# Kernel optimization log

Hardware: AMD Instinct MI355X
Metric: run time of the kernel (lower is better)

## Reference

```python
import jax, jax.numpy as jnp
import numpy as np

N_NODES = 50000
N_EDGES = 800000
D_IN = 128
D_HID = 128
N_LAYERS = 3
BN_EPS = 1e-5


def setup_inputs() -> dict:
    key = jax.random.key(0)
    ks = jax.random.split(key, 12)
    x = jax.random.normal(ks[0], (N_NODES, D_IN), dtype=jnp.float32)
    edge_index = jax.random.randint(ks[1], (2, N_EDGES), 0, N_NODES, dtype=jnp.int64)
    edge_weight = jax.random.uniform(ks[2], (N_EDGES,), dtype=jnp.float32)
    s1 = 1.0 / np.sqrt(D_IN)
    s2 = 1.0 / np.sqrt(D_HID)
    # stacked per-layer GIN MLP params (layer 0 in_dim == hidden_dim so stacking is valid)
    W1s = jax.random.uniform(ks[3], (N_LAYERS, D_HID, D_HID), jnp.float32, -s1, s1)
    b1s = jax.random.uniform(ks[4], (N_LAYERS, D_HID), jnp.float32, -s1, s1)
    W2s = jax.random.uniform(ks[5], (N_LAYERS, D_HID, D_HID), jnp.float32, -s2, s2)
    b2s = jax.random.uniform(ks[6], (N_LAYERS, D_HID), jnp.float32, -s2, s2)
    eps = jnp.zeros((N_LAYERS,), jnp.float32)  # GINConv eps init 0
    gamma = jnp.ones((D_HID,), jnp.float32)
    beta = jnp.zeros((D_HID,), jnp.float32)
    Wp = jax.random.uniform(ks[7], (D_HID, D_HID), jnp.float32, -s2, s2)
    bp = jax.random.uniform(ks[8], (D_HID,), jnp.float32, -s2, s2)
    prelu_a = jnp.asarray(0.25, jnp.float32)
    return {"x": x, "edge_weight": edge_weight, "W1s": W1s, "b1s": b1s,
            "W2s": W2s, "b2s": b2s, "eps": eps, "gamma": gamma, "beta": beta,
            "Wp": Wp, "bp": bp, "prelu_a": prelu_a, "edge_index": edge_index}


def reference(x, edge_weight, W1s, b1s, W2s, b2s, eps, gamma, beta, Wp, bp, prelu_a, edge_index):
    src, dst = edge_index[0], edge_index[1]
    z = x
    for i in range(N_LAYERS):
        # GINConv: sum-aggregate weighted neighbor messages, then 2-layer MLP
        msg = z[src] * edge_weight[:, None]                       # [E, d]
        agg = jax.ops.segment_sum(msg, dst, num_segments=N_NODES)  # [N, d]
        h = (1.0 + eps[i]) * z + agg
        h = jax.nn.relu(h @ W1s[i] + b1s[i]) @ W2s[i] + b2s[i]
        z = jax.nn.relu(h)  # activation; dropout inactive (eval)
    # BatchNorm1d (training-mode batch statistics, biased variance)
    mean = jnp.mean(z, axis=0)
    var = jnp.var(z, axis=0)
    zn = (z - mean) * jax.lax.rsqrt(var + BN_EPS) * gamma + beta
    # projection head: Linear -> PReLU (dropout inactive)
    p = zn @ Wp + bp
    p = jnp.where(p >= 0, p, prelu_a * p)
    return zn, p
```

## Files before the change

kernel.cpp:

```cpp
#include <hip/hip_runtime.h>
#include <hip/hip_fp16.h>

#define N_NODES 50000
#define N_EDGES 800000
#define D 128
#define ND (N_NODES * D)
#define BN_EPS 1e-5f

typedef short bf16x8 __attribute__((ext_vector_type(8)));
typedef float f32x4 __attribute__((ext_vector_type(4)));
typedef unsigned short u16x8 __attribute__((ext_vector_type(8)));

__device__ inline unsigned short f2bf(float f) {
    unsigned int u = __float_as_uint(f);
    u += 0x7FFF + ((u >> 16) & 1);
    return (unsigned short)(u >> 16);
}
__device__ inline float bf2f(unsigned short h) {
    return __uint_as_float(((unsigned int)h) << 16);
}
__device__ inline unsigned short f2h(float f) {
    return __half_as_ushort(__float2half(f));
}
__device__ inline float h2f(unsigned short u) {
    return __half2float(__ushort_as_half(u));
}

__global__ void convert_x(const float* __restrict__ x, ushort* __restrict__ xh) {
    int i = (blockIdx.x * blockDim.x + threadIdx.x) * 4;
    if (i < ND) {
        float4 v = *(const float4*)(x + i);
        *(ushort4*)(xh + i) = make_ushort4(f2h(v.x), f2h(v.y), f2h(v.z), f2h(v.w));
    }
}

__global__ void pack_w_split(const float* __restrict__ W1s, const float* __restrict__ W2s,
                             const float* __restrict__ Wp, ushort* __restrict__ out) {
    int idx = blockIdx.x * blockDim.x + threadIdx.x;
    if (idx >= 7 * 16384) return;
    int m = idx >> 14;
    int p = idx & 16383;
    int c = p >> 11;
    int kc = (p >> 9) & 3;
    int lane = (p >> 3) & 63;
    int j = p & 7;
    int k = kc * 32 + (lane >> 4) * 8 + j;
    int col = c * 16 + (lane & 15);
    const float* src = (m < 3) ? (W1s + (size_t)m * 16384)
                     : (m < 6) ? (W2s + (size_t)(m - 3) * 16384)
                               : Wp;
    float v = src[k * 128 + col];
    unsigned short hi = f2bf(v);
    float r = v - bf2f(hi);
    out[(size_t)(2 * m) * 16384 + p] = hi;
    out[(size_t)(2 * m + 1) * 16384 + p] = f2bf(r);
}

__global__ void hist_kernel(const int* __restrict__ dst, int* __restrict__ offs) {
    int e = blockIdx.x * blockDim.x + threadIdx.x;
    if (e < N_EDGES) atomicAdd(&offs[dst[e] + 1], 1);
}

__global__ void scan_kernel(int* __restrict__ offs, int* __restrict__ cursor) {
    __shared__ int wsum[16];
    __shared__ int carry_s;
    int tid = threadIdx.x;
    int lane = tid & 63;
    int wave = tid >> 6;
    if (tid == 0) { carry_s = 0; cursor[0] = 0; }
    __syncthreads();
    for (int base = 1; base <= N_NODES; base += 8192) {
        int i0 = base + tid * 8;
        int v[8];
        #pragma unroll
        for (int k = 0; k < 8; ++k) {
            int idx = i0 + k;
            v[k] = (idx <= N_NODES) ? offs[idx] : 0;
        }
        #pragma unroll
        for (int k = 1; k < 8; ++k) v[k] += v[k - 1];
        int tsum = v[7];
        int x = tsum;
        #pragma unroll
        for (int d = 1; d < 64; d <<= 1) {
            int y = __shfl_up(x, d, 64);
            if (lane >= d) x += y;
        }
        if (lane == 63) wsum[wave] = x;
        __syncthreads();
        if (wave == 0 && lane < 16) {
            int y = wsum[lane];
            #pragma unroll
            for (int d = 1; d < 16; d <<= 1) {
                int t = __shfl_up(y, d, 64);
                if (lane >= d) y += t;
            }
            wsum[lane] = y;
        }
        __syncthreads();
        int waveoff = (wave > 0) ? wsum[wave - 1] : 0;
        int total = wsum[15];
        int add = (x - tsum) + waveoff + carry_s;
        #pragma unroll
        for (int k = 0; k < 8; ++k) {
            int idx = i0 + k;
            if (idx <= N_NODES) {
                int val = v[k] + add;
                offs[idx] = val;
                if (idx < N_NODES) cursor[idx] = val;
            }
        }
        __syncthreads();
        if (tid == 0) carry_s += total;
        __syncthreads();
    }
}

__global__ void fill_kernel(const int* __restrict__ src, const int* __restrict__ dst,
                            const float* __restrict__ ew,
                            int* __restrict__ cursor, uint2* __restrict__ pay) {
    int e = blockIdx.x * blockDim.x + threadIdx.x;
    if (e < N_EDGES) {
        int d = dst[e];
        int p = atomicAdd(&cursor[d], 1);
        pay[p] = make_uint2((unsigned)src[e], __float_as_uint(ew[e]));
    }
}

__global__ void gather_agg_f16(const ushort* __restrict__ z, const int* __restrict__ offs,
                               const uint2* __restrict__ pay,
                               const float* __restrict__ epsp, int layer,
                               ushort* __restrict__ A) {
    int tid = blockIdx.x * blockDim.x + threadIdx.x;
    int n = tid >> 5;
    if (n >= N_NODES) return;
    int f = (tid & 31) << 2;
    float epsv = 1.0f + epsp[layer];
    int beg = offs[n], end = offs[n + 1];
    ushort4 zi = *(const ushort4*)(z + (size_t)n * D + f);
    float ax = epsv * h2f(zi.x), ay = epsv * h2f(zi.y);
    float az = epsv * h2f(zi.z), aw = epsv * h2f(zi.w);
    int j = beg;
    for (; j + 4 <= end; j += 4) {
        uint2 e0 = pay[j];
        uint2 e1 = pay[j + 1];
        uint2 e2 = pay[j + 2];
        uint2 e3 = pay[j + 3];
        ushort4 v0 = *(const ushort4*)(z + (size_t)e0.x * D + f);
        ushort4 v1 = *(const ushort4*)(z + (size_t)e1.x * D + f);
        ushort4 v2 = *(const ushort4*)(z + (size_t)e2.x * D + f);
        ushort4 v3 = *(const ushort4*)(z + (size_t)e3.x * D + f);
        float w0 = __uint_as_float(e0.y);
        float w1 = __uint_as_float(e1.y);
        float w2 = __uint_as_float(e2.y);
        float w3 = __uint_as_float(e3.y);
        ax += h2f(v0.x) * w0 + h2f(v1.x) * w1 + h2f(v2.x) * w2 + h2f(v3.x) * w3;
        ay += h2f(v0.y) * w0 + h2f(v1.y) * w1 + h2f(v2.y) * w2 + h2f(v3.y) * w3;
        az += h2f(v0.z) * w0 + h2f(v1.z) * w1 + h2f(v2.z) * w2 + h2f(v3.z) * w3;
        aw += h2f(v0.w) * w0 + h2f(v1.w) * w1 + h2f(v2.w) * w2 + h2f(v3.w) * w3;
    }
    for (; j < end; ++j) {
        uint2 e0 = pay[j];
        ushort4 v0 = *(const ushort4*)(z + (size_t)e0.x * D + f);
        float w0 = __uint_as_float(e0.y);
        ax += h2f(v0.x) * w0; ay += h2f(v0.y) * w0;
        az += h2f(v0.z) * w0; aw += h2f(v0.w) * w0;
    }
    *(ushort4*)(A + (size_t)n * D + f) = make_ushort4(f2h(ax), f2h(ay), f2h(az), f2h(aw));
}

#define HSTR 132
template<bool STATS>
__global__ __launch_bounds__(256) void mlp_fused(
    const ushort* __restrict__ A,
    const ushort* __restrict__ W1hi, const ushort* __restrict__ W1lo,
    const float* __restrict__ b1,
    const ushort* __restrict__ W2hi, const ushort* __restrict__ W2lo,
    const float* __restrict__ b2, ushort* __restrict__ Z,
    float* __restrict__ stats) {
    __shared__ float Hs[4][16 * HSTR];
    __shared__ float red[256];
    int tid = threadIdx.x;
    int lane = tid & 63;
    int wave = tid >> 6;
    int rlo = lane & 15;
    int quad = lane >> 4;
    int blk0 = blockIdx.x * 64;
    int row0 = blk0 + wave * 16;
    int arow = row0 + rlo;
    int ar = (arow < N_NODES) ? arow : (N_NODES - 1);

    const bf16x8* W1h = (const bf16x8*)W1hi;
    const bf16x8* W1l = (const bf16x8*)W1lo;
    const bf16x8* W2h = (const bf16x8*)W2hi;
    const bf16x8* W2l = (const bf16x8*)W2lo;

    bf16x8 ahi[4], alo[4];
    #pragma unroll
    for (int kc = 0; kc < 4; ++kc) {
        u16x8 raw = *(const u16x8*)(A + (size_t)ar * D + kc * 32 + quad * 8);
        #pragma unroll
        for (int j = 0; j < 8; ++j) {
            float v = h2f(raw[j]);
            unsigned short h = f2bf(v);
            ahi[kc][j] = (short)h;
            alo[kc][j] = (short)f2bf(v - bf2f(h));
        }
    }

    f32x4 acc[8];
    #pragma unroll
    for (int c = 0; c < 8; ++c) acc[c] = (f32x4){0.f, 0.f, 0.f, 0.f};
    #pragma unroll
    for (int c = 0; c < 8; ++c) {
        #pragma unroll
        for (int kc = 0; kc < 4; ++kc) {
            bf16x8 wh = W1h[(c * 4 + kc) * 64 + lane];
            bf16x8 wl = W1l[(c * 4 + kc) * 64 + lane];
            acc[c] = __builtin_amdgcn_mfma_f32_16x16x32_bf16(alo[kc], wh, acc[c], 0, 0, 0);
            acc[c] = __builtin_amdgcn_mfma_f32_16x16x32_bf16(ahi[kc], wl, acc[c], 0, 0, 0);
            acc[c] = __builtin_amdgcn_mfma_f32_16x16x32_bf16(ahi[kc], wh, acc[c], 0, 0, 0);
        }
    }

    #pragma unroll
    for (int c = 0; c < 8; ++c) {
        int col = c * 16 + rlo;
        float bb = b1[col];
        #pragma unroll
        for (int r = 0; r < 4; ++r) {
            Hs[wave][(quad * 4 + r) * HSTR + col] = fmaxf(acc[c][r] + bb, 0.f);
        }
    }
    __syncthreads();

    bf16x8 a2hi[4], a2lo[4];
    #pragma unroll
    for (int kc = 0; kc < 4; ++kc) {
        const float* p = &Hs[wave][rlo * HSTR + kc * 32 + quad * 8];
        #pragma unroll
        for (int j = 0; j < 8; ++j) {
            float v = p[j];
            unsigned short h = f2bf(v);
            a2hi[kc][j] = (short)h;
            a2lo[kc][j] = (short)f2bf(v - bf2f(h));
        }
    }

    f32x4 acc2[8];
    #pragma unroll
    for (int c = 0; c < 8; ++c) acc2[c] = (f32x4){0.f, 0.f, 0.f, 0.f};
    #pragma unroll
    for (int c = 0; c < 8; ++c) {
        #pragma unroll
        for (int kc = 0; kc < 4; ++kc) {
            bf16x8 wh = W2h[(c * 4 + kc) * 64 + lane];
            bf16x8 wl = W2l[(c * 4 + kc) * 64 + lane];
            acc2[c] = __builtin_amdgcn_mfma_f32_16x16x32_bf16(a2lo[kc], wh, acc2[c], 0, 0, 0);
            acc2[c] = __builtin_amdgcn_mfma_f32_16x16x32_bf16(a2hi[kc], wl, acc2[c], 0, 0, 0);
            acc2[c] = __builtin_amdgcn_mfma_f32_16x16x32_bf16(a2hi[kc], wh, acc2[c], 0, 0, 0);
        }
    }

    __syncthreads();
    #pragma unroll
    for (int c = 0; c < 8; ++c) {
        int col = c * 16 + rlo;
        float bb = b2[col];
        #pragma unroll
        for (int r = 0; r < 4; ++r) {
            Hs[wave][(quad * 4 + r) * HSTR + col] = fmaxf(acc2[c][r] + bb, 0.f);
        }
    }
    __syncthreads();
    #pragma unroll
    for (int p2 = 0; p2 < 4; ++p2) {
        int r = p2 * 4 + quad;
        int grow = row0 + r;
        if (grow < N_NODES) {
            float4 lo = *(const float4*)&Hs[wave][r * HSTR + rlo * 8];
            float4 hi = *(const float4*)&Hs[wave][r * HSTR + rlo * 8 + 4];
            ushort us[8] = {f2h(lo.x), f2h(lo.y), f2h(lo.z), f2h(lo.w),
                            f2h(hi.x), f2h(hi.y), f2h(hi.z), f2h(hi.w)};
            *(float4*)(Z + (size_t)grow * D + rlo * 8) = *(const float4*)us;
        }
    }

    if (STATS) {
        int col = tid & 127;
        int half = tid >> 7;
        float s = 0.f, s2 = 0.f;
        #pragma unroll
        for (int i = 0; i < 32; ++i) {
            int row = half * 32 + i;
            if (blk0 + row < N_NODES) {
                float v = Hs[row >> 4][(row & 15) * HSTR + col];
                s += v;
                s2 += v * v;
            }
        }
        red[tid] = s;
        __syncthreads();
        if (half == 0) atomicAdd(&stats[col], s + red[tid + 128]);
        __syncthreads();
        red[tid] = s2;
        __syncthreads();
        if (half == 0) atomicAdd(&stats[D + col], s2 + red[tid + 128]);
    }
}

#define PSTR 132
__global__ __launch_bounds__(256) void bn_proj(
    const ushort* __restrict__ Z, const float* __restrict__ stats,
    const float* __restrict__ gamma, const float* __restrict__ beta,
    const ushort* __restrict__ Wphi, const ushort* __restrict__ Wplo,
    const float* __restrict__ bp, const float* __restrict__ prelu_a,
    float* __restrict__ zn_out, float* __restrict__ p_out) {
    __shared__ float sc_s[D];
    __shared__ float sh_s[D];
    __shared__ float Ps[4][16 * PSTR];
    int tid = threadIdx.x;
    int lane = tid & 63;
    int wave = tid >> 6;
    int rlo = lane & 15;
    int quad = lane >> 4;

    if (tid < D) {
        float m = stats[tid] * (1.0f / N_NODES);
        float v = stats[D + tid] * (1.0f / N_NODES) - m * m;
        float rs = rsqrtf(v + BN_EPS);
        float sc = rs * gamma[tid];
        sc_s[tid] = sc;
        sh_s[tid] = beta[tid] - m * sc;
    }
    __syncthreads();

    int row0 = blockIdx.x * 64 + wave * 16;
    int arow = row0 + rlo;
    int ar = (arow < N_NODES) ? arow : (N_NODES - 1);

    const bf16x8* Wh = (const bf16x8*)Wphi;
    const bf16x8* Wl = (const bf16x8*)Wplo;

    bf16x8 ahi[4], alo[4];
    #pragma unroll
    for (int kc = 0; kc < 4; ++kc) {
        u16x8 raw = *(const u16x8*)(Z + (size_t)ar * D + kc * 32 + quad * 8);
        float zn[8];
        #pragma unroll
        for (int j = 0; j < 8; ++j) {
            int k = kc * 32 + quad * 8 + j;
            zn[j] = sc_s[k] * h2f(raw[j]) + sh_s[k];
            unsigned short h = f2bf(zn[j]);
            ahi[kc][j] = (short)h;
            alo[kc][j] = (short)f2bf(zn[j] - bf2f(h));
        }
        if (arow < N_NODES) {
            float* dst = zn_out + (size_t)arow * D + kc * 32 + quad * 8;
            *(float4*)dst = make_float4(zn[0], zn[1], zn[2], zn[3]);
            *(float4*)(dst + 4) = make_float4(zn[4], zn[5], zn[6], zn[7]);
        }
    }

    f32x4 acc[8];
    #pragma unroll
    for (int c = 0; c < 8; ++c) acc[c] = (f32x4){0.f, 0.f, 0.f, 0.f};
    #pragma unroll
    for (int c = 0; c < 8; ++c) {
        #pragma unroll
        for (int kc = 0; kc < 4; ++kc) {
            bf16x8 wh = Wh[(c * 4 + kc) * 64 + lane];
            bf16x8 wl = Wl[(c * 4 + kc) * 64 + lane];
            acc[c] = __builtin_amdgcn_mfma_f32_16x16x32_bf16(alo[kc], wh, acc[c], 0, 0, 0);
            acc[c] = __builtin_amdgcn_mfma_f32_16x16x32_bf16(ahi[kc], wl, acc[c], 0, 0, 0);
            acc[c] = __builtin_amdgcn_mfma_f32_16x16x32_bf16(ahi[kc], wh, acc[c], 0, 0, 0);
        }
    }

    float aP = prelu_a[0];
    #pragma unroll
    for (int c = 0; c < 8; ++c) {
        int col = c * 16 + rlo;
        float bb = bp[col];
        #pragma unroll
        for (int r = 0; r < 4; ++r) {
            float v = acc[c][r] + bb;
            v = (v >= 0.f) ? v : aP * v;
            Ps[wave][(quad * 4 + r) * PSTR + col] = v;
        }
    }
    __syncthreads();
    #pragma unroll
    for (int p2 = 0; p2 < 8; ++p2) {
        int r = p2 * 2 + (lane >> 5);
        int grow = row0 + r;
        if (grow < N_NODES) {
            *(float4*)(p_out + (size_t)grow * D + (lane & 31) * 4) =
                *(const float4*)&Ps[wave][r * PSTR + (lane & 31) * 4];
        }
    }
}

extern "C" void kernel_launch(void* const* d_in, const int* in_sizes, int n_in,
                              void* d_out, int out_size, void* d_ws, size_t ws_size,
                              hipStream_t stream) {
    (void)in_sizes; (void)n_in; (void)out_size; (void)ws_size;
    const float* x     = (const float*)d_in[0];
    const float* ew    = (const float*)d_in[1];
    const float* W1s   = (const float*)d_in[2];
    const float* b1s   = (const float*)d_in[3];
    const float* W2s   = (const float*)d_in[4];
    const float* b2s   = (const float*)d_in[5];
    const float* eps   = (const float*)d_in[6];
    const float* gamma = (const float*)d_in[7];
    const float* beta  = (const float*)d_in[8];
    const float* Wp    = (const float*)d_in[9];
    const float* bp    = (const float*)d_in[10];
    const float* pa    = (const float*)d_in[11];
    const int*   ei    = (const int*)d_in[12];
    const int* srcp = ei;
    const int* dstp = ei + N_EDGES;

    char* wsb = (char*)d_ws;
    float*  stats  = (float*)wsb;                 wsb += 1024;
    int*    offs   = (int*)wsb;                   wsb += 200016;
    int*    cursor = (int*)wsb;                   wsb += 200016;
    uint2*  pay    = (uint2*)wsb;                 wsb += 6400000;
    ushort* Wpk    = (ushort*)wsb;                wsb += 14 * 16384 * 2;
    ushort* Xh     = (ushort*)wsb;                wsb += (size_t)ND * 2;
    ushort* Ah     = (ushort*)wsb;                wsb += (size_t)ND * 2;
    ushort* Zh     = (ushort*)wsb;                wsb += (size_t)ND * 2;

    float* out_zn = (float*)d_out;
    float* out_p  = out_zn + ND;

    hipMemsetAsync(stats, 0, 256 * sizeof(float), stream);
    hipMemsetAsync(offs, 0, (N_NODES + 1) * sizeof(int), stream);

    convert_x<<<(ND / 4 + 255) / 256, 256, 0, stream>>>(x, Xh);
    pack_w_split<<<(7 * 16384 + 255) / 256, 256, 0, stream>>>(W1s, W2s, Wp, Wpk);

    hist_kernel<<<(N_EDGES + 255) / 256, 256, 0, stream>>>(dstp, offs);
    scan_kernel<<<1, 1024, 0, stream>>>(offs, cursor);
    fill_kernel<<<(N_EDGES + 255) / 256, 256, 0, stream>>>(srcp, dstp, ew, cursor, pay);

    int mgrid = (N_NODES + 63) / 64;
    const ushort* zin = Xh;
    for (int l = 0; l < 3; ++l) {
        gather_agg_f16<<<(N_NODES * 32 + 255) / 256, 256, 0, stream>>>(zin, offs, pay, eps, l, Ah);
        if (l < 2) {
            mlp_fused<false><<<mgrid, 256, 0, stream>>>(Ah,
                Wpk + (size_t)(2 * l) * 16384,       Wpk + (size_t)(2 * l + 1) * 16384, b1s + (size_t)l * D,
                Wpk + (size_t)(2 * (3 + l)) * 16384, Wpk + (size_t)(2 * (3 + l) + 1) * 16384, b2s + (size_t)l * D,
                Zh, stats);
        } else {
            mlp_fused<true><<<mgrid, 256, 0, stream>>>(Ah,
                Wpk + (size_t)(2 * l) * 16384,       Wpk + (size_t)(2 * l + 1) * 16384, b1s + (size_t)l * D,
                Wpk + (size_t)(2 * (3 + l)) * 16384, Wpk + (size_t)(2 * (3 + l) + 1) * 16384, b2s + (size_t)l * D,
                Zh, stats);
        }
        zin = Zh;
    }
    bn_proj<<<mgrid, 256, 0, stream>>>(Zh, stats, gamma, beta,
        Wpk + (size_t)12 * 16384, Wpk + (size_t)13 * 16384, bp, pa, out_zn, out_p);
}
```

Measured before the change: 438.8 us.

## Switch split-bf16 GEMMs to fp16 activations with scaled hi/lo fp16 weights

```diff
diff --git a/kernel.cpp b/kernel.cpp
--- a/kernel.cpp
+++ b/kernel.cpp
@@ -6,19 +6,13 @@
 #define D 128
 #define ND (N_NODES * D)
 #define BN_EPS 1e-5f
-
-typedef short bf16x8 __attribute__((ext_vector_type(8)));
+#define LO_SCALE 2048.0f
+#define LO_INV (1.0f / 2048.0f)
+
+typedef _Float16 f16x8 __attribute__((ext_vector_type(8)));
 typedef float f32x4 __attribute__((ext_vector_type(4)));
 typedef unsigned short u16x8 __attribute__((ext_vector_type(8)));
 
-__device__ inline unsigned short f2bf(float f) {
-    unsigned int u = __float_as_uint(f);
-    u += 0x7FFF + ((u >> 16) & 1);
-    return (unsigned short)(u >> 16);
-}
-__device__ inline float bf2f(unsigned short h) {
-    return __uint_as_float(((unsigned int)h) << 16);
-}
 __device__ inline unsigned short f2h(float f) {
     return __half_as_ushort(__float2half(f));
 }
@@ -50,10 +44,10 @@
                      : (m < 6) ? (W2s + (size_t)(m - 3) * 16384)
                                : Wp;
     float v = src[k * 128 + col];
-    unsigned short hi = f2bf(v);
-    float r = v - bf2f(hi);
+    unsigned short hi = f2h(v);
+    float r = (v - h2f(hi)) * LO_SCALE;
     out[(size_t)(2 * m) * 16384 + p] = hi;
-    out[(size_t)(2 * m + 1) * 16384 + p] = f2bf(r);
+    out[(size_t)(2 * m + 1) * 16384 + p] = f2h(r);
 }
 
 __global__ void hist_kernel(const int* __restrict__ dst, int* __restrict__ offs) {
@@ -169,7 +163,7 @@
     *(ushort4*)(A + (size_t)n * D + f) = make_ushort4(f2h(ax), f2h(ay), f2h(az), f2h(aw));
 }
 
-#define HSTR 132
+#define HSH 136
 template<bool STATS>
 __global__ __launch_bounds__(256) void mlp_fused(
     const ushort* __restrict__ A,
@@ -178,7 +172,7 @@
     const ushort* __restrict__ W2hi, const ushort* __restrict__ W2lo,
     const float* __restrict__ b2, ushort* __restrict__ Z,
     float* __restrict__ stats) {
-    __shared__ float Hs[4][16 * HSTR];
+    __shared__ ushort Hs[4][16 * HSH];
     __shared__ float red[256];
     int tid = threadIdx.x;
     int lane = tid & 63;
@@ -190,36 +184,25 @@
     int arow = row0 + rlo;
     int ar = (arow < N_NODES) ? arow : (N_NODES - 1);
 
-    const bf16x8* W1h = (const bf16x8*)W1hi;
-    const bf16x8* W1l = (const bf16x8*)W1lo;
-    const bf16x8* W2h = (const bf16x8*)W2hi;
-    const bf16x8* W2l = (const bf16x8*)W2lo;
-
-    bf16x8 ahi[4], alo[4];
-    #pragma unroll
-    for (int kc = 0; kc < 4; ++kc) {
-        u16x8 raw = *(const u16x8*)(A + (size_t)ar * D + kc * 32 + quad * 8);
-        #pragma unroll
-        for (int j = 0; j < 8; ++j) {
-            float v = h2f(raw[j]);
-            unsigned short h = f2bf(v);
-            ahi[kc][j] = (short)h;
-            alo[kc][j] = (short)f2bf(v - bf2f(h));
-        }
-    }
-
-    f32x4 acc[8];
-    #pragma unroll
-    for (int c = 0; c < 8; ++c) acc[c] = (f32x4){0.f, 0.f, 0.f, 0.f};
+    const f16x8* W1h = (const f16x8*)W1hi;
+    const f16x8* W1l = (const f16x8*)W1lo;
+    const f16x8* W2h = (const f16x8*)W2hi;
+    const f16x8* W2l = (const f16x8*)W2lo;
+
+    f16x8 a[4];
+    #pragma unroll
+    for (int kc = 0; kc < 4; ++kc)
+        a[kc] = *(const f16x8*)(A + (size_t)ar * D + kc * 32 + quad * 8);
+
+    f32x4 accH[8], accL[8];
+    #pragma unroll
+    for (int c = 0; c < 8; ++c) { accH[c] = (f32x4){0.f,0.f,0.f,0.f}; accL[c] = (f32x4){0.f,0.f,0.f,0.f}; }
     #pragma unroll
     for (int c = 0; c < 8; ++c) {
         #pragma unroll
         for (int kc = 0; kc < 4; ++kc) {
-            bf16x8 wh = W1h[(c * 4 + kc) * 64 + lane];
-            bf16x8 wl = W1l[(c * 4 + kc) * 64 + lane];
-            acc[c] = __builtin_amdgcn_mfma_f32_16x16x32_bf16(alo[kc], wh, acc[c], 0, 0, 0);
-            acc[c] = __builtin_amdgcn_mfma_f32_16x16x32_bf16(ahi[kc], wl, acc[c], 0, 0, 0);
-            acc[c] = __builtin_amdgcn_mfma_f32_16x16x32_bf16(ahi[kc], wh, acc[c], 0, 0, 0);
+            accH[c] = __builtin_amdgcn_mfma_f32_16x16x32_f16(a[kc], W1h[(c * 4 + kc) * 64 + lane], accH[c], 0, 0, 0);
+            accL[c] = __builtin_amdgcn_mfma_f32_16x16x32_f16(a[kc], W1l[(c * 4 + kc) * 64 + lane], accL[c], 0, 0, 0);
         }
     }
 
@@ -229,64 +212,51 @@
         float bb = b1[col];
         #pragma unroll
         for (int r = 0; r < 4; ++r) {
-            Hs[wave][(quad * 4 + r) * HSTR + col] = fmaxf(acc[c][r] + bb, 0.f);
-        }
-    }
-    __syncthreads();
-
-    bf16x8 a2hi[4], a2lo[4];
-    #pragma unroll
-    for (int kc = 0; kc < 4; ++kc) {
-        const float* p = &Hs[wave][rlo * HSTR + kc * 32 + quad * 8];
-        #pragma unroll
-        for (int j = 0; j < 8; ++j) {
-            float v = p[j];
-            unsigned short h = f2bf(v);
-            a2hi[kc][j] = (short)h;
-            a2lo[kc][j] = (short)f2bf(v - bf2f(h));
-        }
-    }
-
-    f32x4 acc2[8];
-    #pragma unroll
-    for (int c = 0; c < 8; ++c) acc2[c] = (f32x4){0.f, 0.f, 0.f, 0.f};
+            float h = fmaxf(accH[c][r] + accL[c][r] * LO_INV + bb, 0.f);
+            Hs[wave][(quad * 4 + r) * HSH + col] = f2h(h);
+        }
+    }
+
+    f16x8 a2[4];
+    #pragma unroll
+    for (int kc = 0; kc < 4; ++kc)
+        a2[kc] = *(const f16x8*)&Hs[wave][rlo * HSH + kc * 32 + quad * 8];
+
+    f32x4 acc2H[8], acc2L[8];
+    #pragma unroll
+    for (int c = 0; c < 8; ++c) { acc2H[c] = (f32x4){0.f,0.f,0.f,0.f}; acc2L[c] = (f32x4){0.f,0.f,0.f,0.f}; }
     #pragma unroll
     for (int c = 0; c < 8; ++c) {
         #pragma unroll
         for (int kc = 0; kc < 4; ++kc) {
-            bf16x8 wh = W2h[(c * 4 + kc) * 64 + lane];
-            bf16x8 wl = W2l[(c * 4 + kc) * 64 + lane];
-            acc2[c] = __builtin_amdgcn_mfma_f32_16x16x32_bf16(a2lo[kc], wh, acc2[c], 0, 0, 0);
-            acc2[c] = __builtin_amdgcn_mfma_f32_16x16x32_bf16(a2hi[kc], wl, acc2[c], 0, 0, 0);
-            acc2[c] = __builtin_amdgcn_mfma_f32_16x16x32_bf16(a2hi[kc], wh, acc2[c], 0, 0, 0);
-        }
-    }
-
-    __syncthreads();
+            acc2H[c] = __builtin_amdgcn_mfma_f32_16x16x32_f16(a2[kc], W2h[(c * 4 + kc) * 64 + lane], acc2H[c], 0, 0, 0);
+            acc2L[c] = __builtin_amdgcn_mfma_f32_16x16x32_f16(a2[kc], W2l[(c * 4 + kc) * 64 + lane], acc2L[c], 0, 0, 0);
+        }
+    }
+
     #pragma unroll
     for (int c = 0; c < 8; ++c) {
         int col = c * 16 + rlo;
         float bb = b2[col];
         #pragma unroll
         for (int r = 0; r < 4; ++r) {
-            Hs[wave][(quad * 4 + r) * HSTR + col] = fmaxf(acc2[c][r] + bb, 0.f);
-        }
-    }
-    __syncthreads();
+            float z = fmaxf(acc2H[c][r] + acc2L[c][r] * LO_INV + bb, 0.f);
+            Hs[wave][(quad * 4 + r) * HSH + col] = f2h(z);
+        }
+    }
+
     #pragma unroll
     for (int p2 = 0; p2 < 4; ++p2) {
         int r = p2 * 4 + quad;
         int grow = row0 + r;
         if (grow < N_NODES) {
-            float4 lo = *(const float4*)&Hs[wave][r * HSTR + rlo * 8];
-            float4 hi = *(const float4*)&Hs[wave][r * HSTR + rlo * 8 + 4];
-            ushort us[8] = {f2h(lo.x), f2h(lo.y), f2h(lo.z), f2h(lo.w),
-                            f2h(hi.x), f2h(hi.y), f2h(hi.z), f2h(hi.w)};
-            *(float4*)(Z + (size_t)grow * D + rlo * 8) = *(const float4*)us;
+            *(float4*)(Z + (size_t)grow * D + rlo * 8) =
+                *(const float4*)&Hs[wave][r * HSH + rlo * 8];
         }
     }
 
     if (STATS) {
+        __syncthreads();
         int col = tid & 127;
         int half = tid >> 7;
         float s = 0.f, s2 = 0.f;
@@ -294,7 +264,7 @@
         for (int i = 0; i < 32; ++i) {
             int row = half * 32 + i;
             if (blk0 + row < N_NODES) {
-                float v = Hs[row >> 4][(row & 15) * HSTR + col];
+                float v = h2f(Hs[row >> 4][(row & 15) * HSH + col]);
                 s += v;
                 s2 += v * v;
             }
@@ -339,10 +309,10 @@
     int arow = row0 + rlo;
     int ar = (arow < N_NODES) ? arow : (N_NODES - 1);
 
-    const bf16x8* Wh = (const bf16x8*)Wphi;
-    const bf16x8* Wl = (const bf16x8*)Wplo;
-
-    bf16x8 ahi[4], alo[4];
+    const f16x8* Wh = (const f16x8*)Wphi;
+    const f16x8* Wl = (const f16x8*)Wplo;
+
+    f16x8 a[4];
     #pragma unroll
     for (int kc = 0; kc < 4; ++kc) {
         u16x8 raw = *(const u16x8*)(Z + (size_t)ar * D + kc * 32 + quad * 8);
@@ -351,9 +321,7 @@
         for (int j = 0; j < 8; ++j) {
             int k = kc * 32 + quad * 8 + j;
             zn[j] = sc_s[k] * h2f(raw[j]) + sh_s[k];
-            unsigned short h = f2bf(zn[j]);
-            ahi[kc][j] = (short)h;
-            alo[kc][j] = (short)f2bf(zn[j] - bf2f(h));
+            a[kc][j] = (_Float16)zn[j];
         }
         if (arow < N_NODES) {
             float* dst = zn_out + (size_t)arow * D + kc * 32 + quad * 8;
@@ -362,18 +330,15 @@
         }
     }
 
-    f32x4 acc[8];
-    #pragma unroll
-    for (int c = 0; c < 8; ++c) acc[c] = (f32x4){0.f, 0.f, 0.f, 0.f};
+    f32x4 accH[8], accL[8];
+    #pragma unroll
+    for (int c = 0; c < 8; ++c) { accH[c] = (f32x4){0.f,0.f,0.f,0.f}; accL[c] = (f32x4){0.f,0.f,0.f,0.f}; }
     #pragma unroll
     for (int c = 0; c < 8; ++c) {
         #pragma unroll
         for (int kc = 0; kc < 4; ++kc) {
-            bf16x8 wh = Wh[(c * 4 + kc) * 64 + lane];
-            bf16x8 wl = Wl[(c * 4 + kc) * 64 + lane];
-            acc[c] = __builtin_amdgcn_mfma_f32_16x16x32_bf16(alo[kc], wh, acc[c], 0, 0, 0);
-            acc[c] = __builtin_amdgcn_mfma_f32_16x16x32_bf16(ahi[kc], wl, acc[c], 0, 0, 0);
-            acc[c] = __builtin_amdgcn_mfma_f32_16x16x32_bf16(ahi[kc], wh, acc[c], 0, 0, 0);
+            accH[c] = __builtin_amdgcn_mfma_f32_16x16x32_f16(a[kc], Wh[(c * 4 + kc) * 64 + lane], accH[c], 0, 0, 0);
+            accL[c] = __builtin_amdgcn_mfma_f32_16x16x32_f16(a[kc], Wl[(c * 4 + kc) * 64 + lane], accL[c], 0, 0, 0);
         }
     }
 
@@ -384,12 +349,11 @@
         float bb = bp[col];
         #pragma unroll
         for (int r = 0; r < 4; ++r) {
-            float v = acc[c][r] + bb;
+            float v = accH[c][r] + accL[c][r] * LO_INV + bb;
             v = (v >= 0.f) ? v : aP * v;
             Ps[wave][(quad * 4 + r) * PSTR + col] = v;
         }
     }
-    __syncthreads();
     #pragma unroll
     for (int p2 = 0; p2 < 8; ++p2) {
         int r = p2 * 2 + (lane >> 5);
```

Result: slower. 482.8 us (+10.0%).
